# Kernel optimization log

Hardware: AMD Instinct MI355X
Metric: run time of the kernel (lower is better)

Reference implementation:

```python
import jax, jax.numpy as jnp
import numpy as np

K_SIZE = 5  # neighborhood window

def _extract_patches(x, k):
    # tf.image.extract_patches with stride 1, SAME (zero) padding.
    # x: [B,H,W,C] -> [B,H,W,k*k,C]
    pad = k // 2
    B, H, W, C = x.shape
    xp = jnp.pad(x, ((0, 0), (pad, pad), (pad, pad), (0, 0)))
    # fixed small k*k loop (25 shifted views), stacked along patch axis
    return jnp.stack([xp[:, i:i + H, j:j + W, :]
                      for i in range(k) for j in range(k)], axis=3)

def setup_inputs() -> dict:
    key = jax.random.key(0)
    k1, k2, k3 = jax.random.split(key, 3)
    B, H, W, C, BIN = 2, 256, 256, 32, 32
    return {
        "main": jax.random.normal(k1, (B, H, W, C), dtype=jnp.float32),
        "ref": jax.random.normal(k2, (B, H, W, C), dtype=jnp.float32),
        "ref_value": jax.random.normal(k3, (B, H, W, BIN), dtype=jnp.float32),
    }

def reference(main, ref, ref_value):
    # mode='dot': local-window dot-product attention
    ref_stacked = _extract_patches(ref, K_SIZE)          # [B,H,W,k*k,C]
    attn = jnp.einsum('bhwc,bhwkc->bhwk', main, ref_stacked)
    attn = jax.nn.softmax(attn, axis=-1)                 # [B,H,W,k*k]
    # aggregate_mode='weighted_sum'
    ref_value_stacked = _extract_patches(ref_value, K_SIZE)  # [B,H,W,k*k,bin]
    return jnp.einsum('bhwk,bhwki->bhwi', attn, ref_value_stacked)
```

## Files before the change

### kernel.cpp

```cpp
#include <hip/hip_runtime.h>


__global__ void __launch_bounds__(256)
local_attn_kernel(const float* __restrict__ main_p,
                  const float* __restrict__ ref_p,
                  const float* __restrict__ rv_p,
                  float* __restrict__ out_p)
{
    const int lane = threadIdx.x & 63;
    const int wv   = threadIdx.x >> 6;
    const int cg   = lane & 7;
    const int pw   = lane >> 3;
    const int p    = (blockIdx.x * 4 + wv) * 8 + pw;

    const int rem   = p & 65535;
    const int h     = rem >> 8;
    const int w     = rem & 255;
    const int bbase = p - rem;

    const float4* m4 = (const float4*)main_p;
    const float4* r4 = (const float4*)ref_p;
    const float4* v4 = (const float4*)rv_p;
    float4*       o4 = (float4*)out_p;

    const float4 m = m4[p * 8 + cg];

    float  sum = 0.0f;
    float4 acc = make_float4(0.f, 0.f, 0.f, 0.f);

#pragma unroll
    for (int i = 0; i < 5; ++i) {
        const int  hh   = h + i - 2;
        const bool hok  = ((unsigned)hh < 256u);
        const int  rowb = bbase + min(max(hh, 0), 255) * 256;
#pragma unroll
        for (int j = 0; j < 5; ++j) {
            const int  ww   = w + j - 2;
            const bool ok   = hok && ((unsigned)ww < 256u);
            const float msk = ok ? 1.0f : 0.0f;
            const int  np   = rowb + min(max(ww, 0), 255);
            const int  a    = np * 8 + cg;

            const float4 r = r4[a];
            float s = m.x * r.x + m.y * r.y + m.z * r.z + m.w * r.w;
            s += __shfl_xor(s, 1, 64);
            s += __shfl_xor(s, 2, 64);
            s += __shfl_xor(s, 4, 64);

            const float e = __expf(s * msk);
            sum += e;

            const float4 v = v4[a];
            const float wk = e * msk;
            acc.x += wk * v.x; acc.y += wk * v.y;
            acc.z += wk * v.z; acc.w += wk * v.w;
        }
    }

    const float inv = 1.0f / sum;
    acc.x *= inv; acc.y *= inv; acc.z *= inv; acc.w *= inv;
    o4[p * 8 + cg] = acc;
}

extern "C" void kernel_launch(void* const* d_in, const int* in_sizes, int n_in,
                              void* d_out, int out_size, void* d_ws, size_t ws_size,
                              hipStream_t stream)
{
    const float* main_p = (const float*)d_in[0];
    const float* ref_p  = (const float*)d_in[1];
    const float* rv_p   = (const float*)d_in[2];
    float*       out_p  = (float*)d_out;

    const int npix   = in_sizes[0] / 32;
    const int blocks = npix / 32;
    local_attn_kernel<<<blocks, 256, 0, stream>>>(main_p, ref_p, rv_p, out_p);
}
```

Before: 106.1 us.

## Process vertical strips of four pixels per thread to reuse neighbor rows

Result: slower. 132.3 us (+24.7%).

```diff
diff --git a/kernel.cpp b/kernel.cpp
--- a/kernel.cpp
+++ b/kernel.cpp
@@ -1,5 +1,7 @@
 #include <hip/hip_runtime.h>
 
+
+#define STRIP 4
 
 __global__ void __launch_bounds__(256)
 local_attn_kernel(const float* __restrict__ main_p,
@@ -7,59 +9,93 @@
                   const float* __restrict__ rv_p,
                   float* __restrict__ out_p)
 {
-    const int lane = threadIdx.x & 63;
-    const int wv   = threadIdx.x >> 6;
+    const int tid  = threadIdx.x;
+    const int lane = tid & 63;
+    const int wv   = tid >> 6;
     const int cg   = lane & 7;
     const int pw   = lane >> 3;
-    const int p    = (blockIdx.x * 4 + wv) * 8 + pw;
 
-    const int rem   = p & 65535;
-    const int h     = rem >> 8;
-    const int w     = rem & 255;
-    const int bbase = p - rem;
+    const int bid = blockIdx.x;
+    const int cb  = bid & 7;
+    const int rb  = (bid >> 3) & 63;
+    const int b   = bid >> 9;
+
+    const int w   = cb * 32 + wv * 8 + pw;
+    const int hb  = rb * STRIP;
+    const int ib  = b << 16;
 
     const float4* m4 = (const float4*)main_p;
     const float4* r4 = (const float4*)ref_p;
     const float4* v4 = (const float4*)rv_p;
     float4*       o4 = (float4*)out_p;
 
-    const float4 m = m4[p * 8 + cg];
+    int   cbase[5];
+    float cmask[5];
+#pragma unroll
+    for (int j = 0; j < 5; ++j) {
+        const int wj = w + j - 2;
+        cmask[j] = ((unsigned)wj < 256u) ? 1.0f : 0.0f;
+        const int wc = min(max(wj, 0), 255);
+        cbase[j] = ((ib + wc) << 3) + cg;
+    }
 
-    float  sum = 0.0f;
-    float4 acc = make_float4(0.f, 0.f, 0.f, 0.f);
+    float4 m[STRIP];
+    float4 acc[STRIP];
+    float  sum[STRIP];
+#pragma unroll
+    for (int k = 0; k < STRIP; ++k) {
+        m[k]   = m4[((ib + (hb + k) * 256 + w) << 3) + cg];
+        acc[k] = make_float4(0.f, 0.f, 0.f, 0.f);
+        sum[k] = 0.0f;
+    }
 
 #pragma unroll
-    for (int i = 0; i < 5; ++i) {
-        const int  hh   = h + i - 2;
-        const bool hok  = ((unsigned)hh < 256u);
-        const int  rowb = bbase + min(max(hh, 0), 255) * 256;
+    for (int rr = 0; rr < STRIP + 4; ++rr) {
+        const int   r   = hb + rr - 2;
+        const float rok = ((unsigned)r < 256u) ? 1.0f : 0.0f;
+        const int   rc  = min(max(r, 0), 255);
+        const int   roff = rc << 11;
+
+        float4 rrow[5], vrow[5];
+        float  mj[5];
 #pragma unroll
         for (int j = 0; j < 5; ++j) {
-            const int  ww   = w + j - 2;
-            const bool ok   = hok && ((unsigned)ww < 256u);
-            const float msk = ok ? 1.0f : 0.0f;
-            const int  np   = rowb + min(max(ww, 0), 255);
-            const int  a    = np * 8 + cg;
+            rrow[j] = r4[cbase[j] + roff];
+            vrow[j] = v4[cbase[j] + roff];
+            mj[j]   = cmask[j] * rok;
+        }
 
-            const float4 r = r4[a];
-            float s = m.x * r.x + m.y * r.y + m.z * r.z + m.w * r.w;
-            s += __shfl_xor(s, 1, 64);
-            s += __shfl_xor(s, 2, 64);
-            s += __shfl_xor(s, 4, 64);
+#pragma unroll
+        for (int k = 0; k < STRIP; ++k) {
+            if (k >= rr - 4 && k <= rr) {
+#pragma unroll
+                for (int j = 0; j < 5; ++j) {
+                    float s = m[k].x * rrow[j].x + m[k].y * rrow[j].y
+                            + m[k].z * rrow[j].z + m[k].w * rrow[j].w;
+                    s += __shfl_xor(s, 1, 64);
+                    s += __shfl_xor(s, 2, 64);
+                    s += __shfl_xor(s, 4, 64);
 
-            const float e = __expf(s * msk);
-            sum += e;
-
-            const float4 v = v4[a];
-            const float wk = e * msk;
-            acc.x += wk * v.x; acc.y += wk * v.y;
-            acc.z += wk * v.z; acc.w += wk * v.w;
+                    const float e = __expf(s * mj[j]);
+                    sum[k] += e;
+                    const float t = e * mj[j];
+                    acc[k].x += t * vrow[j].x;
+                    acc[k].y += t * vrow[j].y;
+                    acc[k].z += t * vrow[j].z;
+                    acc[k].w += t * vrow[j].w;
+                }
+            }
         }
     }
 
-    const float inv = 1.0f / sum;
-    acc.x *= inv; acc.y *= inv; acc.z *= inv; acc.w *= inv;
-    o4[p * 8 + cg] = acc;
+#pragma unroll
+    for (int k = 0; k < STRIP; ++k) {
+        const float inv = 1.0f / sum[k];
+        float4 o;
+        o.x = acc[k].x * inv; o.y = acc[k].y * inv;
+        o.z = acc[k].z * inv; o.w = acc[k].w * inv;
+        o4[((ib + (hb + k) * 256 + w) << 3) + cg] = o;
+    }
 }
 
 extern "C" void kernel_launch(void* const* d_in, const int* in_sizes, int n_in,
@@ -72,6 +108,6 @@
     float*       out_p  = (float*)d_out;
 
     const int npix   = in_sizes[0] / 32;
-    const int blocks = npix / 32;
+    const int blocks = npix / (32 * STRIP);
     local_attn_kernel<<<blocks, 256, 0, stream>>>(main_p, ref_p, rv_p, out_p);
 }
```

## Stage ref and value rows in double-buffered shared memory tiles

Applied to the files above, without the earlier changes.

Result: faster. 102.0 us (-3.9%).

```diff
diff --git a/kernel.cpp b/kernel.cpp
--- a/kernel.cpp
+++ b/kernel.cpp
@@ -1,5 +1,14 @@
 #include <hip/hip_runtime.h>
 
+
+typedef float v2f __attribute__((ext_vector_type(2)));
+
+template <int CTRL>
+__device__ __forceinline__ float dpp_add(float x)
+{
+    const int y = __builtin_amdgcn_mov_dpp(__float_as_int(x), CTRL, 0xF, 0xF, true);
+    return x + __int_as_float(y);
+}
 
 __global__ void __launch_bounds__(256)
 local_attn_kernel(const float* __restrict__ main_p,
@@ -7,59 +16,133 @@
                   const float* __restrict__ rv_p,
                   float* __restrict__ out_p)
 {
-    const int lane = threadIdx.x & 63;
-    const int wv   = threadIdx.x >> 6;
-    const int cg   = lane & 7;
-    const int pw   = lane >> 3;
-    const int p    = (blockIdx.x * 4 + wv) * 8 + pw;
+    const int tid  = threadIdx.x;
+    const int lane = tid & 63;
+    const int wv   = tid >> 6;
+    const int s    = lane & 3;
+    const int pw   = lane >> 2;
 
-    const int rem   = p & 65535;
-    const int h     = rem >> 8;
-    const int w     = rem & 255;
-    const int bbase = p - rem;
+    const int bid  = blockIdx.x;
+    const int ct   = bid & 15;
+    const int band = (bid >> 4) & 63;
+    const int b    = bid >> 10;
+
+    const int col0 = ct * 16;
+    const int hb   = band * 4;
+    const int ib   = b << 16;
+
+    const int wcol = col0 + pw;
+    const int prow = hb + wv;
 
     const float4* m4 = (const float4*)main_p;
     const float4* r4 = (const float4*)ref_p;
     const float4* v4 = (const float4*)rv_p;
     float4*       o4 = (float4*)out_p;
 
-    const float4 m = m4[p * 8 + cg];
+    __shared__ float4 smem[2][320];
 
-    float  sum = 0.0f;
-    float4 acc = make_float4(0.f, 0.f, 0.f, 0.f);
+    const bool has2 = (tid < 64);
+    int pos0, pos1; const float4 *sp0, *sp1;
+    {
+        const int cc0  = (tid < 160) ? tid : tid - 160;
+        const int col_0 = cc0 >> 3, u0 = cc0 & 7;
+        pos0 = ((tid < 160) ? 0 : 160) + col_0 * 8 + ((u0 + col_0) & 7);
+        const int g0 = min(max(col0 - 2 + col_0, 0), 255);
+        sp0 = ((tid < 160) ? r4 : v4) + (((ib + g0) << 3) + u0);
+
+        const int cc1  = (has2 ? tid : 0) + 96;
+        const int col_1 = cc1 >> 3, u1 = cc1 & 7;
+        pos1 = 160 + col_1 * 8 + ((u1 + col_1) & 7);
+        const int g1 = min(max(col0 - 2 + col_1, 0), 255);
+        sp1 = v4 + (((ib + g1) << 3) + u1);
+    }
+
+    float cmask[5];
+    int   idxA[5], idxB[5];
+#pragma unroll
+    for (int j = 0; j < 5; ++j) {
+        cmask[j] = ((unsigned)(wcol + j - 2) < 256u) ? 1.0f : 0.0f;
+        const int lc = pw + j;
+        idxA[j] = lc * 8 + ((2 * s     + lc) & 7);
+        idxB[j] = lc * 8 + ((2 * s + 1 + lc) & 7);
+    }
+
+    const float L2E = 1.44269504088896340736f;
+
+    v2f mA, mB, mC, mD;
+    {
+        const int pbase = ((ib + prow * 256 + wcol) << 3) + 2 * s;
+        const float4 t0 = m4[pbase];
+        const float4 t1 = m4[pbase + 1];
+        mA = (v2f){t0.x * L2E, t0.y * L2E};
+        mB = (v2f){t0.z * L2E, t0.w * L2E};
+        mC = (v2f){t1.x * L2E, t1.y * L2E};
+        mD = (v2f){t1.z * L2E, t1.w * L2E};
+    }
+    v2f aA = {0.f, 0.f}, aB = {0.f, 0.f}, aC = {0.f, 0.f}, aD = {0.f, 0.f};
+    float sum = 0.0f;
+
+    {
+        const int roff = (min(max(hb - 2, 0), 255)) << 11;
+        smem[0][pos0] = sp0[roff];
+        if (has2) smem[0][pos1] = sp1[roff];
+    }
+    __syncthreads();
+
+#pragma unroll 1
+    for (int rr = 0; rr < 8; ++rr) {
+        float4 st0, st1;
+        const bool more = (rr < 7);
+        if (more) {
+            const int roff = (min(max(hb + rr - 1, 0), 255)) << 11;
+            st0 = sp0[roff];
+            if (has2) st1 = sp1[roff];
+        }
+
+        if (rr >= wv && rr <= wv + 4) {
+            const int   gr  = hb + rr - 2;
+            const float rok = ((unsigned)gr < 256u) ? 1.0f : 0.0f;
+            const float4* bp = &smem[rr & 1][0];
 
 #pragma unroll
-    for (int i = 0; i < 5; ++i) {
-        const int  hh   = h + i - 2;
-        const bool hok  = ((unsigned)hh < 256u);
-        const int  rowb = bbase + min(max(hh, 0), 255) * 256;
-#pragma unroll
-        for (int j = 0; j < 5; ++j) {
-            const int  ww   = w + j - 2;
-            const bool ok   = hok && ((unsigned)ww < 256u);
-            const float msk = ok ? 1.0f : 0.0f;
-            const int  np   = rowb + min(max(ww, 0), 255);
-            const int  a    = np * 8 + cg;
+            for (int j = 0; j < 5; ++j) {
+                const float4 rA4 = bp[idxA[j]];
+                const float4 rB4 = bp[idxB[j]];
+                const float4 vA4 = bp[160 + idxA[j]];
+                const float4 vB4 = bp[160 + idxB[j]];
+                const float  mj  = cmask[j] * rok;
 
-            const float4 r = r4[a];
-            float s = m.x * r.x + m.y * r.y + m.z * r.z + m.w * r.w;
-            s += __shfl_xor(s, 1, 64);
-            s += __shfl_xor(s, 2, 64);
-            s += __shfl_xor(s, 4, 64);
+                v2f p = mA * (v2f){rA4.x, rA4.y};
+                p = mB * (v2f){rA4.z, rA4.w} + p;
+                p = mC * (v2f){rB4.x, rB4.y} + p;
+                p = mD * (v2f){rB4.z, rB4.w} + p;
+                float sc = p.x + p.y;
+                sc = dpp_add<0xB1>(sc);
+                sc = dpp_add<0x4E>(sc);
 
-            const float e = __expf(s * msk);
-            sum += e;
+                const float e = __builtin_exp2f(sc * mj);
+                sum += e;
+                const float t = e * mj;
+                const v2f t2 = {t, t};
+                aA = t2 * (v2f){vA4.x, vA4.y} + aA;
+                aB = t2 * (v2f){vA4.z, vA4.w} + aB;
+                aC = t2 * (v2f){vB4.x, vB4.y} + aC;
+                aD = t2 * (v2f){vB4.z, vB4.w} + aD;
+            }
+        }
 
-            const float4 v = v4[a];
-            const float wk = e * msk;
-            acc.x += wk * v.x; acc.y += wk * v.y;
-            acc.z += wk * v.z; acc.w += wk * v.w;
+        if (more) {
+            const int nb = (rr + 1) & 1;
+            smem[nb][pos0] = st0;
+            if (has2) smem[nb][pos1] = st1;
+            __syncthreads();
         }
     }
 
     const float inv = 1.0f / sum;
-    acc.x *= inv; acc.y *= inv; acc.z *= inv; acc.w *= inv;
-    o4[p * 8 + cg] = acc;
+    const int obase = ((ib + prow * 256 + wcol) << 3) + 2 * s;
+    o4[obase]     = make_float4(aA.x * inv, aA.y * inv, aB.x * inv, aB.y * inv);
+    o4[obase + 1] = make_float4(aC.x * inv, aC.y * inv, aD.x * inv, aD.y * inv);
 }
 
 extern "C" void kernel_launch(void* const* d_in, const int* in_sizes, int n_in,
@@ -72,6 +155,6 @@
     float*       out_p  = (float*)d_out;
 
     const int npix   = in_sizes[0] / 32;
-    const int blocks = npix / 32;
+    const int blocks = npix / 64;
     local_attn_kernel<<<blocks, 256, 0, stream>>>(main_p, ref_p, rv_p, out_p);
 }
```
